# Optimization experiments

Hardware: AMD Instinct MI355X
Metric: run time of the kernel (lower is better)

The kernel has to match this reference:

```python
import jax, jax.numpy as jnp
import numpy as np

N_TYPES = 4
AEV_DIM = 384
HIDDEN = [160, 128, 96]
CELU_ALPHA = 0.1


def _init_params(key):
    dims = [AEV_DIM] + HIDDEN + [1]
    params = {}
    for li in range(len(dims) - 1):
        key, kw = jax.random.split(key)
        scale = 1.0 / np.sqrt(dims[li])
        # stacked over the N_TYPES per-atom-type experts
        params[f"W{li}"] = (jax.random.normal(kw, (N_TYPES, dims[li], dims[li + 1]), dtype=jnp.float32) * scale)
        params[f"b{li}"] = jnp.zeros((N_TYPES, dims[li + 1]), dtype=jnp.float32)
    return params


def setup_inputs() -> dict:
    key = jax.random.key(0)
    k1, k2, k3 = jax.random.split(key, 3)
    B, A = 2048, 64
    species = jax.random.randint(k1, (B, A), 0, N_TYPES, dtype=jnp.int64)
    aev = jax.random.normal(k2, (B, A, AEV_DIM), dtype=jnp.float32)
    inp = {"species": species, "aev": aev}
    inp.update(_init_params(k3))
    return inp


def _mlp(x, t, W0, b0, W1, b1, W2, b2, W3, b3):
    # x: [N, aev_dim] -> [N] per-atom energy for atom type t
    h = jax.nn.celu(x @ W0[t] + b0[t], alpha=CELU_ALPHA)
    h = jax.nn.celu(h @ W1[t] + b1[t], alpha=CELU_ALPHA)
    h = jax.nn.celu(h @ W2[t] + b2[t], alpha=CELU_ALPHA)
    return (h @ W3[t] + b3[t]).reshape(-1)


def reference(species, aev, W0, b0, W1, b1, W2, b2, W3, b3):
    B, A = species.shape
    sp = species.reshape(-1)            # [B*A]
    x = aev.reshape(-1, aev.shape[-1])  # [B*A, aev_dim]
    out = jnp.zeros(sp.shape, dtype=aev.dtype)  # padding_fill = 0
    for t in range(N_TYPES):  # fixed small expert set
        y = _mlp(x, t, W0, b0, W1, b1, W2, b2, W3, b3)
        out = jnp.where(sp == t, y, out)
    energies = out.reshape(B, A).sum(axis=1)  # reduce over atoms
    return species, energies
```

## Files before the change

### kernel.cpp

```cpp
#include <hip/hip_runtime.h>
#include <math.h>


#define NATOMS   131072
#define NMOL     2048
#define AEV      384
#define NTYPES   4
#define MBLK     64
#define PADTOT   (NATOMS + NTYPES * MBLK)
#define NBLK_MLP (PADTOT / MBLK)
#define NBLK_H   512

#define WB_L1 61440
#define WB_L2 81920
#define WB_T  94208

typedef __attribute__((ext_vector_type(8))) short bf16x8;
typedef __attribute__((ext_vector_type(4))) float f32x4;

__device__ __forceinline__ float celu01(float v) {
  return (v > 0.f) ? v : 0.1f * (__expf(v * 10.f) - 1.f);
}
__device__ __forceinline__ unsigned short f2bf(float x) {
  unsigned u = __float_as_uint(x);
  return (unsigned short)((u + 0x7FFFu + ((u >> 16) & 1u)) >> 16);
}
__device__ __forceinline__ unsigned int pk2(float lo, float hi) {
  unsigned a = __float_as_uint(lo), b = __float_as_uint(hi);
  a = (a + 0x7FFFu + ((a >> 16) & 1u)) >> 16;
  b = ((b + 0x7FFFu + ((b >> 16) & 1u)) >> 16) << 16;
  return a | b;
}


__global__ void k_pre(const int* __restrict__ species, float* __restrict__ out,
                      int* __restrict__ perm, int* __restrict__ hist,
                      const float* __restrict__ W0, const float* __restrict__ W1,
                      const float* __restrict__ W2, unsigned short* __restrict__ WB) {
  const int tid = threadIdx.x, blk = blockIdx.x;
  const int i = blk * 256 + tid;
  perm[i] = -1;
  if (i < NATOMS) out[i] = (float)species[i];
  if (i < NMOL) out[NATOMS + i] = 0.f;

  for (int f = i; f < NTYPES * WB_T; f += PADTOT) {
    const int t = f / WB_T, e0 = f - t * WB_T;
    int base, NT, N;
    const float* W;
    if (e0 < WB_L1)      { base = 0;     NT = 10; N = 160; W = W0 + (size_t)t * AEV * 160; }
    else if (e0 < WB_L2) { base = WB_L1; NT = 8;  N = 128; W = W1 + (size_t)t * 160 * 128; }
    else                 { base = WB_L2; NT = 6;  N = 96;  W = W2 + (size_t)t * 128 * 96; }
    const int e = e0 - base, frag = e >> 9, r = e & 511, lane = r >> 3, j = r & 7;
    const int kt = frag / NT, nt = frag - kt * NT;
    const int k = kt * 32 + ((lane >> 4) << 3) + j, n = nt * 16 + (lane & 15);
    WB[(size_t)t * WB_T + e0] = f2bf(W[k * N + n]);
  }

  if (blk < NBLK_H) {
    const int sp = species[i];
    const int wv = tid >> 6;
    __shared__ int wc[4 * NTYPES];
#pragma unroll
    for (int t = 0; t < NTYPES; ++t) {
      const unsigned long long m = __ballot(sp == t);
      if ((tid & 63) == 0) wc[wv * NTYPES + t] = __popcll(m);
    }
    __syncthreads();
    if (tid < NTYPES)
      hist[tid * NBLK_H + blk] = wc[tid] + wc[4 + tid] + wc[8 + tid] + wc[12 + tid];
  }
}


__global__ void k_scan(const int* __restrict__ hist, int* __restrict__ poff,
                       int* __restrict__ boff) {
  __shared__ int tot[NTYPES], base[NTYPES];
  const int tid = threadIdx.x, wv = tid >> 6, lane = tid & 63;
  int s = 0;
  for (int c = 0; c < 8; ++c) s += hist[wv * NBLK_H + c * 64 + lane];
  for (int off = 32; off; off >>= 1) s += __shfl_down(s, off);
  if (lane == 0) tot[wv] = s;
  __syncthreads();
  if (tid == 0) {
    int acc = 0; poff[0] = 0;
    for (int t = 0; t < NTYPES; ++t) {
      base[t] = acc;
      acc += ((tot[t] + 63) >> 6) << 6;
      poff[t + 1] = acc;
    }
  }
  __syncthreads();
  int carry = base[wv];
  for (int c = 0; c < 8; ++c) {
    const int orig = hist[wv * NBLK_H + c * 64 + lane];
    int v = orig;
    for (int off = 1; off < 64; off <<= 1) {
      const int u = __shfl_up(v, off);
      if (lane >= off) v += u;
    }
    boff[wv * NBLK_H + c * 64 + lane] = carry + v - orig;
    carry += __shfl(v, 63);
  }
}

__global__ void k_scatter(const int* __restrict__ species, const int* __restrict__ boff,
                          int* __restrict__ perm) {
  const int tid = threadIdx.x, blk = blockIdx.x;
  const int i = blk * 256 + tid;
  const int sp = species[i];
  const int wv = tid >> 6;
  __shared__ int wc[4 * NTYPES];
  unsigned long long msel = 0;
#pragma unroll
  for (int t = 0; t < NTYPES; ++t) {
    const unsigned long long m = __ballot(sp == t);
    if ((tid & 63) == 0) wc[wv * NTYPES + t] = __popcll(m);
    if (sp == t) msel = m;
  }
  __syncthreads();
  int woff = 0;
  for (int w = 0; w < wv; ++w) woff += wc[w * NTYPES + sp];
  const int rk = __builtin_amdgcn_mbcnt_hi((unsigned)(msel >> 32),
                 __builtin_amdgcn_mbcnt_lo((unsigned)msel, 0));
  perm[boff[sp * NBLK_H + blk] + woff + rk] = i;
}


__global__ __launch_bounds__(128) void k_mlp(
    const float* __restrict__ aev, const unsigned short* __restrict__ WB,
    const float* __restrict__ b0, const float* __restrict__ b1,
    const float* __restrict__ b2, const float* __restrict__ b3,
    const float* __restrict__ W3,
    const int* __restrict__ poff, const int* __restrict__ perm,
    float* __restrict__ outE)
{
  __shared__ __align__(16) unsigned short H[64 * 168];
  __shared__ int permS[64];

  const int tid  = threadIdx.x;
  const int lane = tid & 63;
  const int wv   = __builtin_amdgcn_readfirstlane(tid >> 6);
  const int quad = lane >> 4, l15 = lane & 15;
  const int slot0 = blockIdx.x * MBLK;

  if (tid < 64) permS[tid] = perm[slot0 + tid];
  int t_ = (slot0 >= poff[1]) + (slot0 >= poff[2]) + (slot0 >= poff[3]);
  if (t_ > 3) t_ = 3;
  const int t = __builtin_amdgcn_readfirstlane(t_);
  __syncthreads();

  const float* rp[2];
#pragma unroll
  for (int mtl = 0; mtl < 2; ++mtl) {
    const int ai = permS[(2 * wv + mtl) * 16 + l15];
    rp[mtl] = aev + (size_t)(ai < 0 ? 0 : ai) * AEV + quad * 8;
  }

  const bf16x8* wb0 = (const bf16x8*)(WB + (size_t)t * WB_T);
  const bf16x8* wb1 = (const bf16x8*)(WB + (size_t)t * WB_T + WB_L1);
  const bf16x8* wb2 = (const bf16x8*)(WB + (size_t)t * WB_T + WB_L2);

  union U8 { unsigned int u[4]; bf16x8 v; };

  f32x4 acc0[10][2];
#pragma unroll
  for (int nt = 0; nt < 10; ++nt) {
    const float b = b0[t * 160 + nt * 16 + l15];
#pragma unroll
    for (int mtl = 0; mtl < 2; ++mtl) acc0[nt][mtl] = (f32x4){b, b, b, b};
  }

  float4 raw[2][2];
#pragma unroll
  for (int mtl = 0; mtl < 2; ++mtl) {
    raw[mtl][0] = *(const float4*)(rp[mtl]);
    raw[mtl][1] = *(const float4*)(rp[mtl] + 4);
  }

  for (int ks = 0; ks < 12; ++ks) {
    bf16x8 a[2];
#pragma unroll
    for (int mtl = 0; mtl < 2; ++mtl) {
      U8 c;
      c.u[0] = pk2(raw[mtl][0].x, raw[mtl][0].y);
      c.u[1] = pk2(raw[mtl][0].z, raw[mtl][0].w);
      c.u[2] = pk2(raw[mtl][1].x, raw[mtl][1].y);
      c.u[3] = pk2(raw[mtl][1].z, raw[mtl][1].w);
      a[mtl] = c.v;
    }
    if (ks < 11) {
#pragma unroll
      for (int mtl = 0; mtl < 2; ++mtl) {
        const float* p = rp[mtl] + (ks + 1) * 32;
        raw[mtl][0] = *(const float4*)p;
        raw[mtl][1] = *(const float4*)(p + 4);
      }
    }
#pragma unroll
    for (int nt = 0; nt < 10; ++nt) {
      const bf16x8 w = wb0[(ks * 10 + nt) * 64 + lane];
#pragma unroll
      for (int mtl = 0; mtl < 2; ++mtl)
        acc0[nt][mtl] = __builtin_amdgcn_mfma_f32_16x16x32_bf16(a[mtl], w, acc0[nt][mtl], 0, 0, 0);
    }
  }
#pragma unroll
  for (int nt = 0; nt < 10; ++nt)
#pragma unroll
    for (int mtl = 0; mtl < 2; ++mtl)
#pragma unroll
      for (int r = 0; r < 4; ++r)
        H[((2 * wv + mtl) * 16 + quad * 4 + r) * 168 + nt * 16 + l15] = f2bf(celu01(acc0[nt][mtl][r]));
  __syncthreads();

  f32x4 acc1[8][2];
#pragma unroll
  for (int nt = 0; nt < 8; ++nt) {
    const float b = b1[t * 128 + nt * 16 + l15];
#pragma unroll
    for (int mtl = 0; mtl < 2; ++mtl) acc1[nt][mtl] = (f32x4){b, b, b, b};
  }
#pragma unroll
  for (int ks = 0; ks < 5; ++ks) {
    bf16x8 a[2];
#pragma unroll
    for (int mtl = 0; mtl < 2; ++mtl)
      a[mtl] = *(const bf16x8*)&H[((2 * wv + mtl) * 16 + l15) * 168 + quad * 8 + ks * 32];
#pragma unroll
    for (int nt = 0; nt < 8; ++nt) {
      const bf16x8 w = wb1[(ks * 8 + nt) * 64 + lane];
#pragma unroll
      for (int mtl = 0; mtl < 2; ++mtl)
        acc1[nt][mtl] = __builtin_amdgcn_mfma_f32_16x16x32_bf16(a[mtl], w, acc1[nt][mtl], 0, 0, 0);
    }
  }
  __syncthreads();
#pragma unroll
  for (int nt = 0; nt < 8; ++nt)
#pragma unroll
    for (int mtl = 0; mtl < 2; ++mtl)
#pragma unroll
      for (int r = 0; r < 4; ++r)
        H[((2 * wv + mtl) * 16 + quad * 4 + r) * 136 + nt * 16 + l15] = f2bf(celu01(acc1[nt][mtl][r]));
  __syncthreads();

  f32x4 acc2[6][2];
#pragma unroll
  for (int nt = 0; nt < 6; ++nt) {
    const float b = b2[t * 96 + nt * 16 + l15];
#pragma unroll
    for (int mtl = 0; mtl < 2; ++mtl) acc2[nt][mtl] = (f32x4){b, b, b, b};
  }
#pragma unroll
  for (int ks = 0; ks < 4; ++ks) {
    bf16x8 a[2];
#pragma unroll
    for (int mtl = 0; mtl < 2; ++mtl)
      a[mtl] = *(const bf16x8*)&H[((2 * wv + mtl) * 16 + l15) * 136 + quad * 8 + ks * 32];
#pragma unroll
    for (int nt = 0; nt < 6; ++nt) {
      const bf16x8 w = wb2[(ks * 6 + nt) * 64 + lane];
#pragma unroll
      for (int mtl = 0; mtl < 2; ++mtl)
        acc2[nt][mtl] = __builtin_amdgcn_mfma_f32_16x16x32_bf16(a[mtl], w, acc2[nt][mtl], 0, 0, 0);
    }
  }
  __syncthreads();
#pragma unroll
  for (int nt = 0; nt < 6; ++nt)
#pragma unroll
    for (int mtl = 0; mtl < 2; ++mtl)
#pragma unroll
      for (int r = 0; r < 4; ++r)
        H[((2 * wv + mtl) * 16 + quad * 4 + r) * 104 + nt * 16 + l15] = f2bf(celu01(acc2[nt][mtl][r]));
  __syncthreads();

  bf16x8 w3f[3];
#pragma unroll
  for (int ks = 0; ks < 3; ++ks) {
    const float* wp = W3 + t * 96 + ks * 32 + quad * 8;
    const float4 f0 = *(const float4*)wp;
    const float4 f1 = *(const float4*)(wp + 4);
    U8 c;
    c.u[0] = pk2(f0.x, f0.y);
    c.u[1] = pk2(f0.z, f0.w);
    c.u[2] = pk2(f1.x, f1.y);
    c.u[3] = pk2(f1.z, f1.w);
    w3f[ks] = c.v;
  }
  f32x4 accE[2];
#pragma unroll
  for (int mtl = 0; mtl < 2; ++mtl) accE[mtl] = (f32x4){0.f, 0.f, 0.f, 0.f};
#pragma unroll
  for (int mtl = 0; mtl < 2; ++mtl)
#pragma unroll
    for (int ks = 0; ks < 3; ++ks) {
      const bf16x8 a = *(const bf16x8*)&H[((2 * wv + mtl) * 16 + l15) * 104 + quad * 8 + ks * 32];
      accE[mtl] = __builtin_amdgcn_mfma_f32_16x16x32_bf16(a, w3f[ks], accE[mtl], 0, 0, 0);
    }
  const float bb3 = b3[t];
#pragma unroll
  for (int mtl = 0; mtl < 2; ++mtl)
#pragma unroll
    for (int r = 0; r < 4; ++r)
      if (l15 == 0) {
        const int ai = permS[(2 * wv + mtl) * 16 + quad * 4 + r];
        if (ai >= 0) atomicAdd(&outE[ai >> 6], accE[mtl][r] + bb3);
      }
}


extern "C" void kernel_launch(void* const* d_in, const int* in_sizes, int n_in,
                              void* d_out, int out_size, void* d_ws, size_t ws_size,
                              hipStream_t stream)
{
  const int*   species = (const int*)d_in[0];
  const float* aev     = (const float*)d_in[1];
  const float* W0 = (const float*)d_in[2];
  const float* b0 = (const float*)d_in[3];
  const float* W1 = (const float*)d_in[4];
  const float* b1 = (const float*)d_in[5];
  const float* W2 = (const float*)d_in[6];
  const float* b2 = (const float*)d_in[7];
  const float* W3 = (const float*)d_in[8];
  const float* b3 = (const float*)d_in[9];
  float* out = (float*)d_out;

  int* poff = (int*)d_ws;
  int* hist = poff + 8;
  int* boff = hist + NTYPES * NBLK_H;
  int* perm = boff + NTYPES * NBLK_H;
  unsigned short* WB = (unsigned short*)(perm + PADTOT);

  k_pre    <<<PADTOT / 256, 256, 0, stream>>>(species, out, perm, hist, W0, W1, W2, WB);
  k_scan   <<<1, 256, 0, stream>>>(hist, poff, boff);
  k_scatter<<<NBLK_H, 256, 0, stream>>>(species, boff, perm);
  k_mlp    <<<NBLK_MLP, 128, 0, stream>>>(aev, WB, b0, b1, b2, b3, W3,
                                          poff, perm, out + NATOMS);
}
```

Baseline: 360.2 us.

## Double-buffer weight and activation prefetch across MLP layers, use intrinsic bf16 conversion

Software-pipelines all three hidden layers. Each k-step's weight fragments go into ping-pong register arrays and are loaded one step ahead of the MFMAs that use them, and the fp32 AEV rows are prefetched two steps ahead. The goal is to hide global/L2 load latency behind matrix-core work. It also replaces the manual bf16 rounding with the __float22bfloat162_rn intrinsic, which may map to a packed hardware convert, and adds a launch-bounds min-blocks hint of 2. The extra live registers (up to 20 weight vectors plus 4 float4s) increase register pressure and could reduce occupancy.

Result: slower. 401.7 us (+11.5%).

```diff
diff --git a/kernel.cpp b/kernel.cpp
--- a/kernel.cpp
+++ b/kernel.cpp
@@ -1,4 +1,5 @@
 #include <hip/hip_runtime.h>
+#include <hip/hip_bf16.h>
 #include <math.h>
 
 
@@ -26,10 +27,17 @@
   return (unsigned short)((u + 0x7FFFu + ((u >> 16) & 1u)) >> 16);
 }
 __device__ __forceinline__ unsigned int pk2(float lo, float hi) {
-  unsigned a = __float_as_uint(lo), b = __float_as_uint(hi);
-  a = (a + 0x7FFFu + ((a >> 16) & 1u)) >> 16;
-  b = ((b + 0x7FFFu + ((b >> 16) & 1u)) >> 16) << 16;
-  return a | b;
+  union { __hip_bfloat162 h; unsigned int u; } c;
+  c.h = __float22bfloat162_rn(make_float2(lo, hi));
+  return c.u;
+}
+__device__ __forceinline__ bf16x8 cvt8(const float4 r0, const float4 r1) {
+  union { unsigned int u[4]; bf16x8 v; } c;
+  c.u[0] = pk2(r0.x, r0.y);
+  c.u[1] = pk2(r0.z, r0.w);
+  c.u[2] = pk2(r1.x, r1.y);
+  c.u[3] = pk2(r1.z, r1.w);
+  return c.v;
 }
 
 
@@ -126,7 +134,7 @@
 }
 
 
-__global__ __launch_bounds__(128) void k_mlp(
+__global__ __launch_bounds__(128, 2) void k_mlp(
     const float* __restrict__ aev, const unsigned short* __restrict__ WB,
     const float* __restrict__ b0, const float* __restrict__ b1,
     const float* __restrict__ b2, const float* __restrict__ b3,
@@ -160,8 +168,6 @@
   const bf16x8* wb1 = (const bf16x8*)(WB + (size_t)t * WB_T + WB_L1);
   const bf16x8* wb2 = (const bf16x8*)(WB + (size_t)t * WB_T + WB_L2);
 
-  union U8 { unsigned int u[4]; bf16x8 v; };
-
   f32x4 acc0[10][2];
 #pragma unroll
   for (int nt = 0; nt < 10; ++nt) {
@@ -170,40 +176,56 @@
     for (int mtl = 0; mtl < 2; ++mtl) acc0[nt][mtl] = (f32x4){b, b, b, b};
   }
 
-  float4 raw[2][2];
-#pragma unroll
-  for (int mtl = 0; mtl < 2; ++mtl) {
-    raw[mtl][0] = *(const float4*)(rp[mtl]);
-    raw[mtl][1] = *(const float4*)(rp[mtl] + 4);
-  }
-
-  for (int ks = 0; ks < 12; ++ks) {
-    bf16x8 a[2];
-#pragma unroll
-    for (int mtl = 0; mtl < 2; ++mtl) {
-      U8 c;
-      c.u[0] = pk2(raw[mtl][0].x, raw[mtl][0].y);
-      c.u[1] = pk2(raw[mtl][0].z, raw[mtl][0].w);
-      c.u[2] = pk2(raw[mtl][1].x, raw[mtl][1].y);
-      c.u[3] = pk2(raw[mtl][1].z, raw[mtl][1].w);
-      a[mtl] = c.v;
-    }
-    if (ks < 11) {
-#pragma unroll
-      for (int mtl = 0; mtl < 2; ++mtl) {
-        const float* p = rp[mtl] + (ks + 1) * 32;
-        raw[mtl][0] = *(const float4*)p;
-        raw[mtl][1] = *(const float4*)(p + 4);
-      }
-    }
-#pragma unroll
-    for (int nt = 0; nt < 10; ++nt) {
-      const bf16x8 w = wb0[(ks * 10 + nt) * 64 + lane];
-#pragma unroll
-      for (int mtl = 0; mtl < 2; ++mtl)
-        acc0[nt][mtl] = __builtin_amdgcn_mfma_f32_16x16x32_bf16(a[mtl], w, acc0[nt][mtl], 0, 0, 0);
-    }
-  }
+  bf16x8 wA[10], wB[10];
+  float4 rA[2][2], rB[2][2];
+#pragma unroll
+  for (int nt = 0; nt < 10; ++nt) wA[nt] = wb0[nt * 64 + lane];
+#pragma unroll
+  for (int m = 0; m < 2; ++m) {
+    rA[m][0] = *(const float4*)(rp[m]);
+    rA[m][1] = *(const float4*)(rp[m] + 4);
+    rB[m][0] = *(const float4*)(rp[m] + 32);
+    rB[m][1] = *(const float4*)(rp[m] + 36);
+  }
+
+#define L0_STEP(KS, WC, WN, RC, PFW, PFR)                                      \
+  {                                                                            \
+    const bf16x8 a0 = cvt8(RC[0][0], RC[0][1]);                                \
+    const bf16x8 a1 = cvt8(RC[1][0], RC[1][1]);                                \
+    if (PFR) {                                                                 \
+      _Pragma("unroll")                                                        \
+      for (int m = 0; m < 2; ++m) {                                            \
+        const float* p = rp[m] + (KS + 2) * 32;                                \
+        RC[m][0] = *(const float4*)p;                                          \
+        RC[m][1] = *(const float4*)(p + 4);                                    \
+      }                                                                        \
+    }                                                                          \
+    if (PFW) {                                                                 \
+      _Pragma("unroll")                                                        \
+      for (int nt = 0; nt < 10; ++nt)                                          \
+        WN[nt] = wb0[((KS + 1) * 10 + nt) * 64 + lane];                        \
+    }                                                                          \
+    _Pragma("unroll")                                                          \
+    for (int nt = 0; nt < 10; ++nt) {                                          \
+      acc0[nt][0] = __builtin_amdgcn_mfma_f32_16x16x32_bf16(a0, WC[nt], acc0[nt][0], 0, 0, 0); \
+      acc0[nt][1] = __builtin_amdgcn_mfma_f32_16x16x32_bf16(a1, WC[nt], acc0[nt][1], 0, 0, 0); \
+    }                                                                          \
+  }
+
+  L0_STEP(0,  wA, wB, rA, 1, 1)
+  L0_STEP(1,  wB, wA, rB, 1, 1)
+  L0_STEP(2,  wA, wB, rA, 1, 1)
+  L0_STEP(3,  wB, wA, rB, 1, 1)
+  L0_STEP(4,  wA, wB, rA, 1, 1)
+  L0_STEP(5,  wB, wA, rB, 1, 1)
+  L0_STEP(6,  wA, wB, rA, 1, 1)
+  L0_STEP(7,  wB, wA, rB, 1, 1)
+  L0_STEP(8,  wA, wB, rA, 1, 1)
+  L0_STEP(9,  wB, wA, rB, 1, 1)
+  L0_STEP(10, wA, wB, rA, 1, 0)
+  L0_STEP(11, wB, wA, rB, 0, 0)
+#undef L0_STEP
+
 #pragma unroll
   for (int nt = 0; nt < 10; ++nt)
 #pragma unroll
@@ -220,20 +242,33 @@
 #pragma unroll
     for (int mtl = 0; mtl < 2; ++mtl) acc1[nt][mtl] = (f32x4){b, b, b, b};
   }
-#pragma unroll
-  for (int ks = 0; ks < 5; ++ks) {
-    bf16x8 a[2];
-#pragma unroll
-    for (int mtl = 0; mtl < 2; ++mtl)
-      a[mtl] = *(const bf16x8*)&H[((2 * wv + mtl) * 16 + l15) * 168 + quad * 8 + ks * 32];
-#pragma unroll
-    for (int nt = 0; nt < 8; ++nt) {
-      const bf16x8 w = wb1[(ks * 8 + nt) * 64 + lane];
-#pragma unroll
-      for (int mtl = 0; mtl < 2; ++mtl)
-        acc1[nt][mtl] = __builtin_amdgcn_mfma_f32_16x16x32_bf16(a[mtl], w, acc1[nt][mtl], 0, 0, 0);
-    }
-  }
+  bf16x8 w1A[8], w1B[8];
+#pragma unroll
+  for (int nt = 0; nt < 8; ++nt) w1A[nt] = wb1[nt * 64 + lane];
+
+#define L1_STEP(KS, WC, WN, PFW)                                               \
+  {                                                                            \
+    const bf16x8 a0 = *(const bf16x8*)&H[((2 * wv + 0) * 16 + l15) * 168 + quad * 8 + (KS) * 32]; \
+    const bf16x8 a1 = *(const bf16x8*)&H[((2 * wv + 1) * 16 + l15) * 168 + quad * 8 + (KS) * 32]; \
+    if (PFW) {                                                                 \
+      _Pragma("unroll")                                                        \
+      for (int nt = 0; nt < 8; ++nt)                                           \
+        WN[nt] = wb1[((KS + 1) * 8 + nt) * 64 + lane];                         \
+    }                                                                          \
+    _Pragma("unroll")                                                          \
+    for (int nt = 0; nt < 8; ++nt) {                                           \
+      acc1[nt][0] = __builtin_amdgcn_mfma_f32_16x16x32_bf16(a0, WC[nt], acc1[nt][0], 0, 0, 0); \
+      acc1[nt][1] = __builtin_amdgcn_mfma_f32_16x16x32_bf16(a1, WC[nt], acc1[nt][1], 0, 0, 0); \
+    }                                                                          \
+  }
+
+  L1_STEP(0, w1A, w1B, 1)
+  L1_STEP(1, w1B, w1A, 1)
+  L1_STEP(2, w1A, w1B, 1)
+  L1_STEP(3, w1B, w1A, 1)
+  L1_STEP(4, w1A, w1B, 0)
+#undef L1_STEP
+
   __syncthreads();
 #pragma unroll
   for (int nt = 0; nt < 8; ++nt)
@@ -251,20 +286,32 @@
 #pragma unroll
     for (int mtl = 0; mtl < 2; ++mtl) acc2[nt][mtl] = (f32x4){b, b, b, b};
   }
-#pragma unroll
-  for (int ks = 0; ks < 4; ++ks) {
-    bf16x8 a[2];
-#pragma unroll
-    for (int mtl = 0; mtl < 2; ++mtl)
-      a[mtl] = *(const bf16x8*)&H[((2 * wv + mtl) * 16 + l15) * 136 + quad * 8 + ks * 32];
-#pragma unroll
-    for (int nt = 0; nt < 6; ++nt) {
-      const bf16x8 w = wb2[(ks * 6 + nt) * 64 + lane];
-#pragma unroll
-      for (int mtl = 0; mtl < 2; ++mtl)
-        acc2[nt][mtl] = __builtin_amdgcn_mfma_f32_16x16x32_bf16(a[mtl], w, acc2[nt][mtl], 0, 0, 0);
-    }
-  }
+  bf16x8 w2A[6], w2B[6];
+#pragma unroll
+  for (int nt = 0; nt < 6; ++nt) w2A[nt] = wb2[nt * 64 + lane];
+
+#define L2_STEP(KS, WC, WN, PFW)                                               \
+  {                                                                            \
+    const bf16x8 a0 = *(const bf16x8*)&H[((2 * wv + 0) * 16 + l15) * 136 + quad * 8 + (KS) * 32]; \
+    const bf16x8 a1 = *(const bf16x8*)&H[((2 * wv + 1) * 16 + l15) * 136 + quad * 8 + (KS) * 32]; \
+    if (PFW) {                                                                 \
+      _Pragma("unroll")                                                        \
+      for (int nt = 0; nt < 6; ++nt)                                           \
+        WN[nt] = wb2[((KS + 1) * 6 + nt) * 64 + lane];                         \
+    }                                                                          \
+    _Pragma("unroll")                                                          \
+    for (int nt = 0; nt < 6; ++nt) {                                           \
+      acc2[nt][0] = __builtin_amdgcn_mfma_f32_16x16x32_bf16(a0, WC[nt], acc2[nt][0], 0, 0, 0); \
+      acc2[nt][1] = __builtin_amdgcn_mfma_f32_16x16x32_bf16(a1, WC[nt], acc2[nt][1], 0, 0, 0); \
+    }                                                                          \
+  }
+
+  L2_STEP(0, w2A, w2B, 1)
+  L2_STEP(1, w2B, w2A, 1)
+  L2_STEP(2, w2A, w2B, 1)
+  L2_STEP(3, w2B, w2A, 0)
+#undef L2_STEP
+
   __syncthreads();
 #pragma unroll
   for (int nt = 0; nt < 6; ++nt)
@@ -281,12 +328,7 @@
     const float* wp = W3 + t * 96 + ks * 32 + quad * 8;
     const float4 f0 = *(const float4*)wp;
     const float4 f1 = *(const float4*)(wp + 4);
-    U8 c;
-    c.u[0] = pk2(f0.x, f0.y);
-    c.u[1] = pk2(f0.z, f0.w);
-    c.u[2] = pk2(f1.x, f1.y);
-    c.u[3] = pk2(f1.z, f1.w);
-    w3f[ks] = c.v;
+    w3f[ks] = cvt8(f0, f1);
   }
   f32x4 accE[2];
 #pragma unroll
```

## Stage bf16 weights into LDS with double-buffered async global_load_lds

Applied to the files above, without the earlier changes.

Weight fragments for all three hidden layers are now copied from global memory into a double-buffered LDS tile with global_load_lds, one k-step ahead of the MFMA loop, instead of being read directly from global per MFMA. This is meant to hide weight-load latency behind compute, and it chains the prefetch across layer boundaries. The fp32-to-bf16 packing also switches to the HIP intrinsic __float22bfloat162_rn. In exchange, the kernel adds a __syncthreads per k-step and uses about 20KB more LDS, which may reduce occupancy. There is also no explicit wait on the async LDS loads before they are consumed, so correctness relies on the barrier ordering.

Result: no change. 367.3 us (+2.0%).

```diff
diff --git a/kernel.cpp b/kernel.cpp
--- a/kernel.cpp
+++ b/kernel.cpp
@@ -1,4 +1,5 @@
 #include <hip/hip_runtime.h>
+#include <hip/hip_bf16.h>
 #include <math.h>
 
 
@@ -26,10 +27,22 @@
   return (unsigned short)((u + 0x7FFFu + ((u >> 16) & 1u)) >> 16);
 }
 __device__ __forceinline__ unsigned int pk2(float lo, float hi) {
-  unsigned a = __float_as_uint(lo), b = __float_as_uint(hi);
-  a = (a + 0x7FFFu + ((a >> 16) & 1u)) >> 16;
-  b = ((b + 0x7FFFu + ((b >> 16) & 1u)) >> 16) << 16;
-  return a | b;
+  union { __hip_bfloat162 h; unsigned int u; } c;
+  c.h = __float22bfloat162_rn(make_float2(lo, hi));
+  return c.u;
+}
+__device__ __forceinline__ bf16x8 cvt8(const float4 r0, const float4 r1) {
+  union { unsigned int u[4]; bf16x8 v; } c;
+  c.u[0] = pk2(r0.x, r0.y);
+  c.u[1] = pk2(r0.z, r0.w);
+  c.u[2] = pk2(r1.x, r1.y);
+  c.u[3] = pk2(r1.z, r1.w);
+  return c.v;
+}
+__device__ __forceinline__ void dma16(const unsigned short* g, unsigned short* l) {
+  __builtin_amdgcn_global_load_lds(
+      (const __attribute__((address_space(1))) void*)(g),
+      (__attribute__((address_space(3))) void*)(l), 16, 0, 0);
 }
 
 
@@ -135,6 +148,7 @@
     float* __restrict__ outE)
 {
   __shared__ __align__(16) unsigned short H[64 * 168];
+  __shared__ __align__(16) unsigned short WL[2][5120];
   __shared__ int permS[64];
 
   const int tid  = threadIdx.x;
@@ -147,6 +161,13 @@
   int t_ = (slot0 >= poff[1]) + (slot0 >= poff[2]) + (slot0 >= poff[3]);
   if (t_ > 3) t_ = 3;
   const int t = __builtin_amdgcn_readfirstlane(t_);
+
+  const unsigned short* WBt = WB + (size_t)t * WB_T;
+
+#pragma unroll
+  for (int s = 0; s < 5; ++s)
+    dma16(WBt + (wv * 5 + s) * 512 + lane * 8, &WL[0][(wv * 5 + s) * 512]);
+
   __syncthreads();
 
   const float* rp[2];
@@ -156,12 +177,6 @@
     rp[mtl] = aev + (size_t)(ai < 0 ? 0 : ai) * AEV + quad * 8;
   }
 
-  const bf16x8* wb0 = (const bf16x8*)(WB + (size_t)t * WB_T);
-  const bf16x8* wb1 = (const bf16x8*)(WB + (size_t)t * WB_T + WB_L1);
-  const bf16x8* wb2 = (const bf16x8*)(WB + (size_t)t * WB_T + WB_L2);
-
-  union U8 { unsigned int u[4]; bf16x8 v; };
-
   f32x4 acc0[10][2];
 #pragma unroll
   for (int nt = 0; nt < 10; ++nt) {
@@ -178,16 +193,9 @@
   }
 
   for (int ks = 0; ks < 12; ++ks) {
-    bf16x8 a[2];
-#pragma unroll
-    for (int mtl = 0; mtl < 2; ++mtl) {
-      U8 c;
-      c.u[0] = pk2(raw[mtl][0].x, raw[mtl][0].y);
-      c.u[1] = pk2(raw[mtl][0].z, raw[mtl][0].w);
-      c.u[2] = pk2(raw[mtl][1].x, raw[mtl][1].y);
-      c.u[3] = pk2(raw[mtl][1].z, raw[mtl][1].w);
-      a[mtl] = c.v;
-    }
+    const int cur = ks & 1;
+    const bf16x8 a0 = cvt8(raw[0][0], raw[0][1]);
+    const bf16x8 a1 = cvt8(raw[1][0], raw[1][1]);
     if (ks < 11) {
 #pragma unroll
       for (int mtl = 0; mtl < 2; ++mtl) {
@@ -195,15 +203,25 @@
         raw[mtl][0] = *(const float4*)p;
         raw[mtl][1] = *(const float4*)(p + 4);
       }
+#pragma unroll
+      for (int s = 0; s < 5; ++s)
+        dma16(WBt + ((ks + 1) * 10 + wv * 5 + s) * 512 + lane * 8,
+              &WL[cur ^ 1][(wv * 5 + s) * 512]);
+    } else {
+#pragma unroll
+      for (int s = 0; s < 4; ++s)
+        dma16(WBt + WB_L1 + (wv * 4 + s) * 512 + lane * 8,
+              &WL[cur ^ 1][(wv * 4 + s) * 512]);
     }
 #pragma unroll
     for (int nt = 0; nt < 10; ++nt) {
-      const bf16x8 w = wb0[(ks * 10 + nt) * 64 + lane];
-#pragma unroll
-      for (int mtl = 0; mtl < 2; ++mtl)
-        acc0[nt][mtl] = __builtin_amdgcn_mfma_f32_16x16x32_bf16(a[mtl], w, acc0[nt][mtl], 0, 0, 0);
-    }
-  }
+      const bf16x8 w = *(const bf16x8*)&WL[cur][nt * 512 + lane * 8];
+      acc0[nt][0] = __builtin_amdgcn_mfma_f32_16x16x32_bf16(a0, w, acc0[nt][0], 0, 0, 0);
+      acc0[nt][1] = __builtin_amdgcn_mfma_f32_16x16x32_bf16(a1, w, acc0[nt][1], 0, 0, 0);
+    }
+    __syncthreads();
+  }
+
 #pragma unroll
   for (int nt = 0; nt < 10; ++nt)
 #pragma unroll
@@ -220,21 +238,29 @@
 #pragma unroll
     for (int mtl = 0; mtl < 2; ++mtl) acc1[nt][mtl] = (f32x4){b, b, b, b};
   }
-#pragma unroll
   for (int ks = 0; ks < 5; ++ks) {
-    bf16x8 a[2];
-#pragma unroll
-    for (int mtl = 0; mtl < 2; ++mtl)
-      a[mtl] = *(const bf16x8*)&H[((2 * wv + mtl) * 16 + l15) * 168 + quad * 8 + ks * 32];
+    const int cur = ks & 1;
+    const bf16x8 a0 = *(const bf16x8*)&H[((2 * wv + 0) * 16 + l15) * 168 + quad * 8 + ks * 32];
+    const bf16x8 a1 = *(const bf16x8*)&H[((2 * wv + 1) * 16 + l15) * 168 + quad * 8 + ks * 32];
+    if (ks < 4) {
+#pragma unroll
+      for (int s = 0; s < 4; ++s)
+        dma16(WBt + WB_L1 + ((ks + 1) * 8 + wv * 4 + s) * 512 + lane * 8,
+              &WL[cur ^ 1][(wv * 4 + s) * 512]);
+    } else {
+#pragma unroll
+      for (int s = 0; s < 3; ++s)
+        dma16(WBt + WB_L2 + (wv * 3 + s) * 512 + lane * 8,
+              &WL[cur ^ 1][(wv * 3 + s) * 512]);
+    }
 #pragma unroll
     for (int nt = 0; nt < 8; ++nt) {
-      const bf16x8 w = wb1[(ks * 8 + nt) * 64 + lane];
-#pragma unroll
-      for (int mtl = 0; mtl < 2; ++mtl)
-        acc1[nt][mtl] = __builtin_amdgcn_mfma_f32_16x16x32_bf16(a[mtl], w, acc1[nt][mtl], 0, 0, 0);
-    }
-  }
-  __syncthreads();
+      const bf16x8 w = *(const bf16x8*)&WL[cur][nt * 512 + lane * 8];
+      acc1[nt][0] = __builtin_amdgcn_mfma_f32_16x16x32_bf16(a0, w, acc1[nt][0], 0, 0, 0);
+      acc1[nt][1] = __builtin_amdgcn_mfma_f32_16x16x32_bf16(a1, w, acc1[nt][1], 0, 0, 0);
+    }
+    __syncthreads();
+  }
 #pragma unroll
   for (int nt = 0; nt < 8; ++nt)
 #pragma unroll
@@ -251,21 +277,24 @@
 #pragma unroll
     for (int mtl = 0; mtl < 2; ++mtl) acc2[nt][mtl] = (f32x4){b, b, b, b};
   }
-#pragma unroll
   for (int ks = 0; ks < 4; ++ks) {
-    bf16x8 a[2];
-#pragma unroll
-    for (int mtl = 0; mtl < 2; ++mtl)
-      a[mtl] = *(const bf16x8*)&H[((2 * wv + mtl) * 16 + l15) * 136 + quad * 8 + ks * 32];
+    const int cur = (ks + 1) & 1;
+    const bf16x8 a0 = *(const bf16x8*)&H[((2 * wv + 0) * 16 + l15) * 136 + quad * 8 + ks * 32];
+    const bf16x8 a1 = *(const bf16x8*)&H[((2 * wv + 1) * 16 + l15) * 136 + quad * 8 + ks * 32];
+    if (ks < 3) {
+#pragma unroll
+      for (int s = 0; s < 3; ++s)
+        dma16(WBt + WB_L2 + ((ks + 1) * 6 + wv * 3 + s) * 512 + lane * 8,
+              &WL[cur ^ 1][(wv * 3 + s) * 512]);
+    }
 #pragma unroll
     for (int nt = 0; nt < 6; ++nt) {
-      const bf16x8 w = wb2[(ks * 6 + nt) * 64 + lane];
-#pragma unroll
-      for (int mtl = 0; mtl < 2; ++mtl)
-        acc2[nt][mtl] = __builtin_amdgcn_mfma_f32_16x16x32_bf16(a[mtl], w, acc2[nt][mtl], 0, 0, 0);
-    }
-  }
-  __syncthreads();
+      const bf16x8 w = *(const bf16x8*)&WL[cur][nt * 512 + lane * 8];
+      acc2[nt][0] = __builtin_amdgcn_mfma_f32_16x16x32_bf16(a0, w, acc2[nt][0], 0, 0, 0);
+      acc2[nt][1] = __builtin_amdgcn_mfma_f32_16x16x32_bf16(a1, w, acc2[nt][1], 0, 0, 0);
+    }
+    __syncthreads();
+  }
 #pragma unroll
   for (int nt = 0; nt < 6; ++nt)
 #pragma unroll
@@ -281,12 +310,7 @@
     const float* wp = W3 + t * 96 + ks * 32 + quad * 8;
     const float4 f0 = *(const float4*)wp;
     const float4 f1 = *(const float4*)(wp + 4);
-    U8 c;
-    c.u[0] = pk2(f0.x, f0.y);
-    c.u[1] = pk2(f0.z, f0.w);
-    c.u[2] = pk2(f1.x, f1.y);
-    c.u[3] = pk2(f1.z, f1.w);
-    w3f[ks] = c.v;
+    w3f[ks] = cvt8(f0, f1);
   }
   f32x4 accE[2];
 #pragma unroll
```
